# Optimization experiments

Hardware: AMD Instinct MI355X
Metric: run time of the kernel (lower is better)

## Reference

```python
import jax, jax.numpy as jnp
import numpy as np

RADIUS = 5
EPS = 1e-08


def _box_blur(x, r):
    """Normalized (2r+1)x(2r+1) box filter with reflect padding, NCHW."""
    k = 2 * r + 1
    B, C, H, W = x.shape
    xp = jnp.pad(x, ((0, 0), (0, 0), (r, r), (r, r)), mode='reflect')
    y = xp.reshape(B * C, 1, H + 2 * r, W + 2 * r)
    kh = jnp.ones((1, 1, k, 1), x.dtype) / k
    kw = jnp.ones((1, 1, 1, k), x.dtype) / k
    y = jax.lax.conv_general_dilated(y, kh, (1, 1), 'VALID')
    y = jax.lax.conv_general_dilated(y, kw, (1, 1), 'VALID')
    return y.reshape(B, C, H, W)


def setup_inputs() -> dict:
    key = jax.random.key(0)
    k1, k2 = jax.random.split(key)
    feat = jax.random.uniform(k1, (8, 16, 512, 512), dtype=jnp.float32)
    img = jax.random.uniform(k2, (8, 1, 512, 512), dtype=jnp.float32)
    return {"feat": feat, "img": img}


def reference(feat, img):
    r, eps = RADIUS, EPS
    # scalar-guidance guided filter (guidance img has 1 channel)
    mean_I = _box_blur(img, r)                  # [B,1,H,W]
    mean_p = _box_blur(feat, r)                 # [B,D,H,W]
    corr_I = _box_blur(img * img, r)            # [B,1,H,W]
    corr_Ip = _box_blur(img * feat, r)          # [B,D,H,W]
    var_I = corr_I - mean_I * mean_I
    cov_Ip = corr_Ip - mean_I * mean_p
    a = cov_Ip / (var_I + eps)                  # [B,D,H,W]
    b = mean_p - a * mean_I                     # [B,D,H,W]
    mean_a = _box_blur(a, r)
    mean_b = _box_blur(b, r)
    return mean_a * img + mean_b
```

## Files before the change

kernel.cpp:

```cpp
#include <hip/hip_runtime.h>

#define HH 512
#define WW 512
#define HW (512*512)
#define NB 8
#define ND 16
#define TW 64
#define TH 32
#define VR 42
#define RAWC 84
#define PT 85

__device__ __forceinline__ int reflect(int v) {
    if (v < 0) v = -v;
    if (v >= HH) v = 2*HH - 2 - v;
    return v;
}

__global__ __launch_bounds__(256) void img_stats(const float* __restrict__ img,
                                                 float* __restrict__ meanI,
                                                 float* __restrict__ invv) {
    const int EE = 42, Q = 43, PH = 33;
    __shared__ float sI[EE*Q], sI2[EE*Q];
    __shared__ float hI[EE*PH], hI2[EE*PH];

    int blk  = blockIdx.x;
    int tile = blk & 255;
    int b    = blk >> 8;
    int ty0  = (tile >> 4) * 32;
    int tx0  = (tile & 15) * 32;
    const float* ib = img + (size_t)b*HW;
    const float inv121 = 1.0f/121.0f;

    for (int i = threadIdx.x; i < EE*EE; i += 256) {
        int y = i / EE, x = i - y*EE;
        int gy = reflect(ty0 - 5 + y);
        int gx = reflect(tx0 - 5 + x);
        float v = ib[gy*WW + gx];
        sI [y*Q + x] = v;
        sI2[y*Q + x] = v*v;
    }
    __syncthreads();
    if (threadIdx.x < 168) {
        int t = threadIdx.x;
        int arr = t / 84, r2 = t - arr*84;
        int seg = r2 / 42, row = r2 - seg*42;
        const float* sr = (arr ? sI2 : sI) + row*Q;
        float* dr = (arr ? hI2 : hI) + row*PH;
        int x0 = seg*16;
        float s = 0.f;
        #pragma unroll
        for (int j = 0; j < 10; ++j) s += sr[x0+j];
        #pragma unroll
        for (int x = 0; x < 16; ++x) {
            s += sr[x0+x+10];
            dr[x0+x] = s;
            s -= sr[x0+x];
        }
    }
    __syncthreads();
    {
        int t = threadIdx.x;
        int arr = t >> 7, r2 = t & 127;
        int seg = r2 >> 5, col = r2 & 31;
        const float* src = arr ? hI2 : hI;
        float* dst = arr ? sI2 : sI;
        int y0 = seg*8;
        float s = 0.f;
        #pragma unroll
        for (int j = 0; j < 10; ++j) s += src[(y0+j)*PH+col];
        #pragma unroll
        for (int k = 0; k < 8; ++k) {
            int y = y0 + k;
            s += src[(y+10)*PH+col];
            dst[y*Q+col] = s;
            s -= src[y*PH+col];
        }
    }
    __syncthreads();
    for (int i = threadIdx.x; i < 32*32; i += 256) {
        int y = i >> 5, x = i & 31;
        float mI  = sI [y*Q+x]*inv121;
        float mII = sI2[y*Q+x]*inv121;
        float var = mII - mI*mI;
        int gy = ty0 + y, gx = tx0 + x;
        meanI[(size_t)b*HW + gy*WW + gx] = mI;
        invv [(size_t)b*HW + gy*WW + gx] = 1.0f / (var + 1e-8f);
    }
}

__global__ __launch_bounds__(256) void guided_main(const float* __restrict__ feat,
                                                   const float* __restrict__ img,
                                                   const float* __restrict__ meanI,
                                                   const float* __restrict__ invv,
                                                   float* __restrict__ out) {
    __shared__ float hF[VR*PT];
    __shared__ float hP[VR*PT];

    int blk  = blockIdx.x;
    int tile = blk & 127;
    int bd   = blk >> 7;
    int b    = bd >> 4;
    int ty0  = (tile >> 3) * TH;
    int tx0  = (tile & 7)  * TW;

    const float inv121 = 1.0f/121.0f;
    const float* fb  = feat  + (size_t)bd*HW;
    const float* ib  = img   + (size_t)b*HW;
    const float* mIb = meanI + (size_t)b*HW;
    const float* ivb = invv  + (size_t)b*HW;
    const int t = threadIdx.x;

    if (t < 252) {
        int seg = t / 84, col = t - seg*84;
        int gx = reflect(tx0 - 10 + col);
        const float* fcol = fb + gx;
        const float* icol = ib + gx;
        int vr0 = seg*14;
        float rf[11], rp[11];
        float sf = 0.f, sp = 0.f;
        #pragma unroll
        for (int j = 0; j < 10; ++j) {
            int gy = reflect(ty0 - 10 + vr0 + j);
            float f = fcol[gy*WW], im = icol[gy*WW];
            float p = f*im;
            rf[j] = f; rp[j] = p; sf += f; sp += p;
        }
        #pragma unroll
        for (int k = 0; k < 14; ++k) {
            int vr = vr0 + k;
            int gy = reflect(ty0 + vr);
            float f = fcol[gy*WW], im = icol[gy*WW];
            float p = f*im;
            sf += f; sp += p;
            hF[vr*PT + col] = sf;
            hP[vr*PT + col] = sp;
            sf -= rf[k%11]; sp -= rp[k%11];
            rf[(k+10)%11] = f; rp[(k+10)%11] = p;
        }
    }
    __syncthreads();

    if (t < 168) {
        int arr = t & 1;
        int j2  = t >> 1;
        int seg = j2 / 42, vr = j2 - seg*42;
        int xb = seg*37;
        float* rA = (arr ? hP : hF) + vr*PT;
        float ring[11];
        float s = 0.f;
        #pragma unroll
        for (int j = 0; j < 10; ++j) {
            float v = rA[xb+j];
            ring[j] = v; s += v;
        }
        #pragma unroll
        for (int k = 0; k < 37; ++k) {
            int hc = xb + k;
            float v = rA[hc+10];
            s += v;
            rA[hc + 10*seg] = s*inv121;
            s -= ring[k%11];
            ring[(k+10)%11] = v;
        }
    }
    __syncthreads();

    for (int i = t; i < VR*74; i += 256) {
        int y = i / 74, x = i - y*74;
        int slot = x + ((x >= 37) ? 10 : 0);
        float mp  = hF[y*PT + slot];
        float cip = hP[y*PT + slot];
        int gy = reflect(ty0 - 5 + y);
        int gx = reflect(tx0 - 5 + x);
        float mI = mIb[gy*WW + gx];
        float iv = ivb[gy*WW + gx];
        float a  = (cip - mI*mp) * iv;
        hF[y*PT + slot] = a;
        hP[y*PT + slot] = mp - a*mI;
    }
    __syncthreads();

    if (t < 148) {
        int arr = t & 1;
        int c   = t >> 1;
        int slotc = c + ((c >= 37) ? 10 : 0);
        float* A = (arr ? hP : hF);
        float ring[11];
        float s = 0.f;
        #pragma unroll
        for (int j = 0; j < 10; ++j) {
            float v = A[j*PT + slotc];
            ring[j] = v; s += v;
        }
        #pragma unroll
        for (int k = 0; k < 32; ++k) {
            float v = A[(k+10)*PT + slotc];
            s += v;
            A[k*PT + slotc] = s;
            s -= ring[k%11];
            ring[(k+10)%11] = v;
        }
    }
    __syncthreads();

    if (t < 128) {
        int arr = t & 1;
        int r2  = t >> 1;
        int seg = r2 >> 5, row = r2 & 31;
        float* rp_ = (arr ? hP : hF) + row*PT;
        int xb = seg*32;
        float ring[11];
        float s = 0.f;
        #pragma unroll
        for (int j = 0; j < 10; ++j) {
            int hc = xb + j;
            int slot = hc + ((hc >= 37) ? 10 : 0);
            float v = rp_[slot];
            ring[j] = v; s += v;
        }
        #pragma unroll
        for (int k = 0; k < 32; ++k) {
            int hc = xb + k + 10;
            int slot = hc + ((hc >= 37) ? 10 : 0);
            float v = rp_[slot];
            s += v;
            int wcol = xb + k + 20*seg;
            rp_[wcol] = s;
            s -= ring[k%11];
            ring[(k+10)%11] = v;
        }
    }
    __syncthreads();

    float* ob = out + (size_t)bd*HW;
    for (int i = t; i < TH*TW; i += 256) {
        int y = i >> 6, x = i & 63;
        int wcol = (x < 32) ? x : x + 20;
        float ma = hF[y*PT + wcol]*inv121;
        float mb = hP[y*PT + wcol]*inv121;
        int gy = ty0 + y, gx = tx0 + x;
        float im = ib[gy*WW + gx];
        ob[gy*WW + gx] = ma*im + mb;
    }
}

extern "C" void kernel_launch(void* const* d_in, const int* in_sizes, int n_in,
                              void* d_out, int out_size, void* d_ws, size_t ws_size,
                              hipStream_t stream) {
    const float* feat = (const float*)d_in[0];
    const float* img  = (const float*)d_in[1];
    float* out   = (float*)d_out;
    float* meanI = (float*)d_ws;
    float* invv  = meanI + (size_t)NB*HW;

    img_stats<<<NB*256, 256, 0, stream>>>(img, meanI, invv);
    guided_main<<<NB*ND*128, 256, 0, stream>>>(feat, img, meanI, invv, out);
}
```

Before: 174.7 us.

## Vectorize guided filter stages with float2 and interleave meanI/invvar buffer

Interleaves the per-pixel mean and inverse variance into one float2 workspace so the main kernel fetches both with a single load. Every stage of guided_main now processes two adjacent columns per thread with float2 global and shared-memory accesses. The shared layout is repartitioned (pitch 86, new segment splits, paired sliding-window sums) to keep those accesses aligned. This halves per-thread load/store instruction counts but raises register use, and the changed segment splits alter thread utilization and bank patterns.

After: 224.8 us. 1.29x slower.

```diff
diff --git a/kernel.cpp b/kernel.cpp
--- a/kernel.cpp
+++ b/kernel.cpp
@@ -8,8 +8,7 @@
 #define TW 64
 #define TH 32
 #define VR 42
-#define RAWC 84
-#define PT 85
+#define PT 86
 
 __device__ __forceinline__ int reflect(int v) {
     if (v < 0) v = -v;
@@ -18,8 +17,7 @@
 }
 
 __global__ __launch_bounds__(256) void img_stats(const float* __restrict__ img,
-                                                 float* __restrict__ meanI,
-                                                 float* __restrict__ invv) {
+                                                 float2* __restrict__ miv) {
     const int EE = 42, Q = 43, PH = 33;
     __shared__ float sI[EE*Q], sI2[EE*Q];
     __shared__ float hI[EE*PH], hI2[EE*PH];
@@ -84,18 +82,17 @@
         float mII = sI2[y*Q+x]*inv121;
         float var = mII - mI*mI;
         int gy = ty0 + y, gx = tx0 + x;
-        meanI[(size_t)b*HW + gy*WW + gx] = mI;
-        invv [(size_t)b*HW + gy*WW + gx] = 1.0f / (var + 1e-8f);
+        float2 o; o.x = mI; o.y = 1.0f / (var + 1e-8f);
+        miv[(size_t)b*HW + gy*WW + gx] = o;
     }
 }
 
 __global__ __launch_bounds__(256) void guided_main(const float* __restrict__ feat,
                                                    const float* __restrict__ img,
-                                                   const float* __restrict__ meanI,
-                                                   const float* __restrict__ invv,
+                                                   const float2* __restrict__ miv,
                                                    float* __restrict__ out) {
-    __shared__ float hF[VR*PT];
-    __shared__ float hP[VR*PT];
+    __shared__ __align__(16) float hF[VR*PT];
+    __shared__ __align__(16) float hP[VR*PT];
 
     int blk  = blockIdx.x;
     int tile = blk & 127;
@@ -105,38 +102,50 @@
     int tx0  = (tile & 7)  * TW;
 
     const float inv121 = 1.0f/121.0f;
-    const float* fb  = feat  + (size_t)bd*HW;
-    const float* ib  = img   + (size_t)b*HW;
-    const float* mIb = meanI + (size_t)b*HW;
-    const float* ivb = invv  + (size_t)b*HW;
+    const float* fb   = feat + (size_t)bd*HW;
+    const float* ib   = img  + (size_t)b*HW;
+    const float2* mivb = miv + (size_t)b*HW;
     const int t = threadIdx.x;
 
     if (t < 252) {
-        int seg = t / 84, col = t - seg*84;
-        int gx = reflect(tx0 - 10 + col);
-        const float* fcol = fb + gx;
-        const float* icol = ib + gx;
-        int vr0 = seg*14;
-        float rf[11], rp[11];
-        float sf = 0.f, sp = 0.f;
+        int seg = t / 42, c2 = t - seg*42;
+        int col0 = 2*c2;
+        int gx0 = tx0 - 10 + col0;
+        bool edge = (gx0 < 0) || (gx0 > WW-2);
+        int rg0 = reflect(gx0), rg1 = reflect(gx0+1);
+        int vr0 = seg*7;
+        float2 rf[11], rp[11];
+        float sfx=0.f, sfy=0.f, spx=0.f, spy=0.f;
         #pragma unroll
         for (int j = 0; j < 10; ++j) {
             int gy = reflect(ty0 - 10 + vr0 + j);
-            float f = fcol[gy*WW], im = icol[gy*WW];
-            float p = f*im;
-            rf[j] = f; rp[j] = p; sf += f; sp += p;
-        }
-        #pragma unroll
-        for (int k = 0; k < 14; ++k) {
+            const float* fr = fb + gy*WW;
+            const float* ir = ib + gy*WW;
+            float2 f2, i2;
+            if (edge) { f2.x = fr[rg0]; f2.y = fr[rg1]; i2.x = ir[rg0]; i2.y = ir[rg1]; }
+            else      { f2 = *(const float2*)(fr + gx0); i2 = *(const float2*)(ir + gx0); }
+            float2 p2; p2.x = f2.x*i2.x; p2.y = f2.y*i2.y;
+            rf[j] = f2; rp[j] = p2;
+            sfx += f2.x; sfy += f2.y; spx += p2.x; spy += p2.y;
+        }
+        #pragma unroll
+        for (int k = 0; k < 7; ++k) {
             int vr = vr0 + k;
             int gy = reflect(ty0 + vr);
-            float f = fcol[gy*WW], im = icol[gy*WW];
-            float p = f*im;
-            sf += f; sp += p;
-            hF[vr*PT + col] = sf;
-            hP[vr*PT + col] = sp;
-            sf -= rf[k%11]; sp -= rp[k%11];
-            rf[(k+10)%11] = f; rp[(k+10)%11] = p;
+            const float* fr = fb + gy*WW;
+            const float* ir = ib + gy*WW;
+            float2 f2, i2;
+            if (edge) { f2.x = fr[rg0]; f2.y = fr[rg1]; i2.x = ir[rg0]; i2.y = ir[rg1]; }
+            else      { f2 = *(const float2*)(fr + gx0); i2 = *(const float2*)(ir + gx0); }
+            float2 p2; p2.x = f2.x*i2.x; p2.y = f2.y*i2.y;
+            sfx += f2.x; sfy += f2.y; spx += p2.x; spy += p2.y;
+            float2 oF; oF.x = sfx; oF.y = sfy;
+            float2 oP; oP.x = spx; oP.y = spy;
+            *(float2*)(&hF[vr*PT + col0]) = oF;
+            *(float2*)(&hP[vr*PT + col0]) = oP;
+            sfx -= rf[k%11].x; sfy -= rf[k%11].y;
+            spx -= rp[k%11].x; spy -= rp[k%11].y;
+            rf[(k+10)%11] = f2; rp[(k+10)%11] = p2;
         }
     }
     __syncthreads();
@@ -144,61 +153,84 @@
     if (t < 168) {
         int arr = t & 1;
         int j2  = t >> 1;
-        int seg = j2 / 42, vr = j2 - seg*42;
-        int xb = seg*37;
+        int seg = (j2 >= 42) ? 1 : 0;
+        int vr  = j2 - seg*42;
+        int xb = seg ? 38 : 0;
+        int nout = seg ? 18 : 19;
         float* rA = (arr ? hP : hF) + vr*PT;
-        float ring[11];
-        float s = 0.f;
-        #pragma unroll
-        for (int j = 0; j < 10; ++j) {
-            float v = rA[xb+j];
-            ring[j] = v; s += v;
-        }
-        #pragma unroll
-        for (int k = 0; k < 37; ++k) {
-            int hc = xb + k;
-            float v = rA[hc+10];
-            s += v;
-            rA[hc + 10*seg] = s*inv121;
-            s -= ring[k%11];
-            ring[(k+10)%11] = v;
-        }
-    }
-    __syncthreads();
-
-    for (int i = t; i < VR*74; i += 256) {
-        int y = i / 74, x = i - y*74;
-        int slot = x + ((x >= 37) ? 10 : 0);
-        float mp  = hF[y*PT + slot];
-        float cip = hP[y*PT + slot];
+        float2 ring[5];
+        float T = 0.f;
+        #pragma unroll
+        for (int j = 0; j < 5; ++j) {
+            float2 v = *(float2*)(rA + xb + 2*j);
+            ring[j] = v; T += v.x + v.y;
+        }
+        #pragma unroll
+        for (int k2 = 0; k2 < 19; ++k2) {
+            if (k2 < nout) {
+                int hc = xb + 2*k2;
+                float2 p = *(float2*)(rA + hc + 10);
+                float2 q = ring[k2 % 5];
+                float O0 = T + p.x;
+                float O1 = O0 + p.y - q.x;
+                T = O1 - q.y;
+                ring[k2 % 5] = p;
+                float2 o; o.x = O0*inv121; o.y = O1*inv121;
+                *(float2*)(rA + hc + 10*seg) = o;
+            }
+        }
+    }
+    __syncthreads();
+
+    for (int i = t; i < VR*37; i += 256) {
+        int y = i / 37, c2 = i - y*37;
+        int x0 = 2*c2;
+        int slot = x0 + ((x0 >= 38) ? 10 : 0);
+        float* pF = &hF[y*PT + slot];
+        float* pP = &hP[y*PT + slot];
+        float2 mp2  = *(float2*)pF;
+        float2 cip2 = *(float2*)pP;
         int gy = reflect(ty0 - 5 + y);
-        int gx = reflect(tx0 - 5 + x);
-        float mI = mIb[gy*WW + gx];
-        float iv = ivb[gy*WW + gx];
-        float a  = (cip - mI*mp) * iv;
-        hF[y*PT + slot] = a;
-        hP[y*PT + slot] = mp - a*mI;
+        const float2* mrow = mivb + gy*WW;
+        int gx0 = tx0 - 5 + x0;
+        float2 g0 = mrow[reflect(gx0)];
+        float2 g1 = mrow[reflect(gx0+1)];
+        float a0 = (cip2.x - g0.x*mp2.x) * g0.y;
+        float b0 = mp2.x - a0*g0.x;
+        float a1 = (cip2.y - g1.x*mp2.y) * g1.y;
+        float b1 = mp2.y - a1*g1.x;
+        float2 oa; oa.x = a0; oa.y = a1;
+        float2 ob2; ob2.x = b0; ob2.y = b1;
+        *(float2*)pF = oa;
+        *(float2*)pP = ob2;
     }
     __syncthreads();
 
     if (t < 148) {
         int arr = t & 1;
-        int c   = t >> 1;
-        int slotc = c + ((c >= 37) ? 10 : 0);
+        int j2  = t >> 1;
+        int seg = (j2 >= 37) ? 1 : 0;
+        int c2  = j2 - seg*37;
+        int x0 = 2*c2;
+        int slotc = x0 + ((x0 >= 38) ? 10 : 0);
+        int y0 = seg*16;
         float* A = (arr ? hP : hF);
-        float ring[11];
-        float s = 0.f;
+        float2 ring[11];
+        float sx = 0.f, sy = 0.f;
         #pragma unroll
         for (int j = 0; j < 10; ++j) {
-            float v = A[j*PT + slotc];
-            ring[j] = v; s += v;
-        }
-        #pragma unroll
-        for (int k = 0; k < 32; ++k) {
-            float v = A[(k+10)*PT + slotc];
-            s += v;
-            A[k*PT + slotc] = s;
-            s -= ring[k%11];
+            float2 v = *(float2*)(A + (y0+j)*PT + slotc);
+            ring[j] = v; sx += v.x; sy += v.y;
+        }
+        #pragma unroll
+        for (int k = 0; k < 16; ++k) {
+            int y = y0 + k;
+            float2 v = *(float2*)(A + (y+10)*PT + slotc);
+            sx += v.x; sy += v.y;
+            int wrow = y + 10*seg;
+            float2 o; o.x = sx; o.y = sy;
+            *(float2*)(A + wrow*PT + slotc) = o;
+            sx -= ring[k%11].x; sy -= ring[k%11].y;
             ring[(k+10)%11] = v;
         }
     }
@@ -208,40 +240,50 @@
         int arr = t & 1;
         int r2  = t >> 1;
         int seg = r2 >> 5, row = r2 & 31;
-        float* rp_ = (arr ? hP : hF) + row*PT;
+        int prow = row + ((row >= 16) ? 10 : 0);
+        float* rA = (arr ? hP : hF) + prow*PT;
         int xb = seg*32;
-        float ring[11];
-        float s = 0.f;
-        #pragma unroll
-        for (int j = 0; j < 10; ++j) {
-            int hc = xb + j;
-            int slot = hc + ((hc >= 37) ? 10 : 0);
-            float v = rp_[slot];
-            ring[j] = v; s += v;
-        }
-        #pragma unroll
-        for (int k = 0; k < 32; ++k) {
-            int hc = xb + k + 10;
-            int slot = hc + ((hc >= 37) ? 10 : 0);
-            float v = rp_[slot];
-            s += v;
-            int wcol = xb + k + 20*seg;
-            rp_[wcol] = s;
-            s -= ring[k%11];
-            ring[(k+10)%11] = v;
+        float2 ring[5];
+        float T = 0.f;
+        #pragma unroll
+        for (int j = 0; j < 5; ++j) {
+            int idx = xb + 2*j;
+            int sl = idx + ((idx >= 38) ? 10 : 0);
+            float2 v = *(float2*)(rA + sl);
+            ring[j] = v; T += v.x + v.y;
+        }
+        #pragma unroll
+        for (int k2 = 0; k2 < 16; ++k2) {
+            int x = xb + 2*k2;
+            int idx = x + 10;
+            int sl = idx + ((idx >= 38) ? 10 : 0);
+            float2 p = *(float2*)(rA + sl);
+            float2 q = ring[k2 % 5];
+            float O0 = T + p.x;
+            float O1 = O0 + p.y - q.x;
+            T = O1 - q.y;
+            ring[k2 % 5] = p;
+            int wcol = x + 20*seg;
+            float2 o; o.x = O0; o.y = O1;
+            *(float2*)(rA + wcol) = o;
         }
     }
     __syncthreads();
 
     float* ob = out + (size_t)bd*HW;
-    for (int i = t; i < TH*TW; i += 256) {
-        int y = i >> 6, x = i & 63;
-        int wcol = (x < 32) ? x : x + 20;
-        float ma = hF[y*PT + wcol]*inv121;
-        float mb = hP[y*PT + wcol]*inv121;
-        int gy = ty0 + y, gx = tx0 + x;
-        float im = ib[gy*WW + gx];
-        ob[gy*WW + gx] = ma*im + mb;
+    for (int i = t; i < TH*32; i += 256) {
+        int y = i >> 5, c2 = i & 31;
+        int x0 = 2*c2;
+        int prow = y + ((y >= 16) ? 10 : 0);
+        int wcol = (x0 < 32) ? x0 : x0 + 20;
+        float2 ma2 = *(float2*)(&hF[prow*PT + wcol]);
+        float2 mb2 = *(float2*)(&hP[prow*PT + wcol]);
+        int gy = ty0 + y;
+        float2 im2 = *(const float2*)(ib + gy*WW + tx0 + x0);
+        float2 o;
+        o.x = (ma2.x*im2.x + mb2.x)*inv121;
+        o.y = (ma2.y*im2.y + mb2.y)*inv121;
+        *(float2*)(ob + gy*WW + tx0 + x0) = o;
     }
 }
 
@@ -250,10 +292,9 @@
                               hipStream_t stream) {
     const float* feat = (const float*)d_in[0];
     const float* img  = (const float*)d_in[1];
-    float* out   = (float*)d_out;
-    float* meanI = (float*)d_ws;
-    float* invv  = meanI + (size_t)NB*HW;
-
-    img_stats<<<NB*256, 256, 0, stream>>>(img, meanI, invv);
-    guided_main<<<NB*ND*128, 256, 0, stream>>>(feat, img, meanI, invv, out);
+    float* out  = (float*)d_out;
+    float2* miv = (float2*)d_ws;
+
+    img_stats<<<NB*256, 256, 0, stream>>>(img, miv);
+    guided_main<<<NB*ND*128, 256, 0, stream>>>(feat, img, miv, out);
 }
```
